# Kernel tuning notes

Measured on AMD Instinct MI355X. Metric: run time of the kernel, lower is better.

The kernel has to match this reference:

```python
import jax, jax.numpy as jnp
import numpy as np

N = 1024                      # FFT length (init kwarg)
NF = N // 2 + 1               # rfft output length = len(freq)
PB_LO = 40.0 / 60.0           # pulse_band[0] in Hz
PB_HI = 180.0 / 60.0          # pulse_band[1] in Hz
DELTA_HZ = 6.0 / 60.0         # self.delta after /60
W0, W1 = 1.0, 1.0             # weights[0], weights[1]
B, T = 32768, 1024


def setup_inputs() -> dict:
    key = jax.random.key(0)
    k1, k2 = jax.random.split(key)
    preds = jax.random.normal(k1, (B, T), dtype=jnp.float32)
    # realistic camera frame rates ~25-35 Hz (must exceed 2*pulse_band[1]=6 Hz)
    Fs = 25.0 + 10.0 * jax.random.uniform(k2, (B,), dtype=jnp.float32)
    return {"preds": preds, "Fs": Fs}


def reference(preds, Fs):
    idx = jnp.arange(NF)                                            # [Nf]
    # freq = linspace(0, Fs/2, Nf) per sample -> [B, Nf]
    freq = (Fs[:, None] * 0.5) * (idx.astype(jnp.float32) / (NF - 1))
    left = jnp.argmin(jnp.abs(freq - PB_LO), axis=1)                # [B] int
    right = jnp.argmin(jnp.abs(freq - PB_HI), axis=1)               # [B] int

    psd = jnp.abs(jnp.fft.rfft(preds, n=N)) ** 2                    # [B, Nf]
    total = jnp.sum(psd, axis=-1)                                   # [B]

    l = left[:, None]
    r = right[:, None]
    out_band = (idx < l) | (idx >= r)                               # psd[:left] + psd[right:]
    band_loss = jnp.sum(jnp.where(out_band, psd, 0.0), axis=-1) / (1e-8 + total)

    in_band = (idx >= l) & (idx < r)
    # argmax(psd[left:right]) + left  (psd >= 0, so -inf mask is safe)
    peak = jnp.argmax(jnp.where(in_band, psd, -jnp.inf), axis=1)    # [B]
    # delta = max(1, round(self.delta / (Fs/2/len(freq))))  (round half-to-even, as Python)
    delta = jnp.maximum(1.0, jnp.round(DELTA_HZ / (Fs * 0.5 / NF))).astype(jnp.int32)

    p = peak[:, None]
    d = delta[:, None]
    # psd[left:peak-delta] + psd[peak+delta:right]  (empty slices -> 0 via mask)
    sparse_mask = in_band & ((idx < p - d) | (idx >= p + d))
    num = jnp.sum(jnp.where(sparse_mask, psd, 0.0), axis=-1)
    # sum(psd[left:right] + 1e-8) adds 1e-8 per in-band bin, keep faithful
    den = jnp.sum(jnp.where(in_band, psd + 1e-8, 0.0), axis=-1)
    sparse_loss = num / den

    return W0 * jnp.mean(band_loss) + W1 * jnp.mean(sparse_loss)
```

## Files before the change

### kernel.cpp

```cpp
#include <hip/hip_runtime.h>
#include <cmath>

#define BATCH 32768

struct cplx { float x, y; };
__device__ __forceinline__ cplx cadd(cplx a, cplx b){ return {a.x+b.x, a.y+b.y}; }
__device__ __forceinline__ cplx csub(cplx a, cplx b){ return {a.x-b.x, a.y-b.y}; }
__device__ __forceinline__ cplx cmul(cplx a, cplx b){ return {a.x*b.x - a.y*b.y, a.x*b.y + a.y*b.x}; }
__device__ __forceinline__ cplx cmul_mi(cplx a){ return {a.y, -a.x}; }
__device__ __forceinline__ cplx cmul_w81(cplx a){ const float c=0.70710678f; return {c*(a.x+a.y), c*(a.y-a.x)}; }
__device__ __forceinline__ cplx cmul_w83(cplx a){ const float c=0.70710678f; return {c*(a.y-a.x), -c*(a.x+a.y)}; }

__device__ __forceinline__ void dft8(cplx a[8]) {
    cplx t0=cadd(a[0],a[4]), t4=csub(a[0],a[4]);
    cplx t1=cadd(a[1],a[5]), t5=csub(a[1],a[5]);
    cplx t2=cadd(a[2],a[6]), t6=csub(a[2],a[6]);
    cplx t3=cadd(a[3],a[7]), t7=csub(a[3],a[7]);
    cplx u0=cadd(t0,t2), u2=csub(t0,t2);
    cplx u1=cadd(t1,t3), u3=cmul_mi(csub(t1,t3));
    a[0]=cadd(u0,u1); a[4]=csub(u0,u1); a[2]=cadd(u2,u3); a[6]=csub(u2,u3);
    cplx v0=t4, v1=cmul_w81(t5), v2=cmul_mi(t6), v3=cmul_w83(t7);
    cplx w0=cadd(v0,v2), w2=csub(v0,v2);
    cplx w1=cadd(v1,v3), w3=cmul_mi(csub(v1,v3));
    a[1]=cadd(w0,w1); a[5]=csub(w0,w1); a[3]=cadd(w2,w3); a[7]=csub(w2,w3);
}

__device__ __forceinline__ int nearest_bin(float fs, float target) {
    float x = target * 1024.0f / fs;
    int i0 = (int)floorf(x);
    int lo = max(0, i0 - 1), hi = min(512, i0 + 2);
    int bi = lo; float bd = 1e30f;
    for (int i = lo; i <= hi; ++i) {
        float fr = (fs * 0.5f) * ((float)i / 512.0f);
        float d = fabsf(fr - target);
        if (d < bd) { bd = d; bi = i; }
    }
    return bi;
}

__global__ __launch_bounds__(256) void fft_loss_kernel(
    const float* __restrict__ preds, const float* __restrict__ Fs,
    float* __restrict__ blockpartial)
{
    __shared__ float sre[4][576];
    __shared__ float sim[4][576];
    __shared__ float sblk[4];

    const int tid  = threadIdx.x;
    const int wv   = tid >> 6;
    const int lane = tid & 63;
    const int row  = blockIdx.x * 4 + wv;

    float* re = sre[wv];
    float* im = sim[wv];

    const float fs = Fs[row];

    const float2* x2 = reinterpret_cast<const float2*>(preds) + (size_t)row * 512;

    cplx z[8];
#pragma unroll
    for (int n1 = 0; n1 < 8; ++n1) {
        float2 v = x2[n1 * 64 + lane];
        z[n1] = {v.x, v.y};
    }
    dft8(z);
    {
        float sb, cb;
        __sincosf(-0.012271846f * (float)lane, &sb, &cb);
        cplx w1 = {cb, sb};
        cplx w2 = cmul(w1, w1);
        cplx w3 = cmul(w2, w1);
        cplx w4 = cmul(w2, w2);
        cplx w5 = cmul(w4, w1);
        cplx w6 = cmul(w4, w2);
        cplx w7 = cmul(w4, w3);
        z[1]=cmul(z[1],w1); z[2]=cmul(z[2],w2); z[3]=cmul(z[3],w3); z[4]=cmul(z[4],w4);
        z[5]=cmul(z[5],w5); z[6]=cmul(z[6],w6); z[7]=cmul(z[7],w7);
    }
#pragma unroll
    for (int r = 0; r < 8; ++r) { re[r*72 + lane] = z[r].x; im[r*72 + lane] = z[r].y; }

    const int rB = lane & 7, m0 = lane >> 3;
    cplx b[8];
#pragma unroll
    for (int m1 = 0; m1 < 8; ++m1) {
        int a = rB*72 + 8*m1 + m0;
        b[m1] = {re[a], im[a]};
    }
    dft8(b);
    {
        float sb, cb;
        __sincosf(-0.09817477f * (float)m0, &sb, &cb);
        cplx w1 = {cb, sb};
        cplx w2 = cmul(w1, w1);
        cplx w3 = cmul(w2, w1);
        cplx w4 = cmul(w2, w2);
        cplx w5 = cmul(w4, w1);
        cplx w6 = cmul(w4, w2);
        cplx w7 = cmul(w4, w3);
        b[1]=cmul(b[1],w1); b[2]=cmul(b[2],w2); b[3]=cmul(b[3],w3); b[4]=cmul(b[4],w4);
        b[5]=cmul(b[5],w5); b[6]=cmul(b[6],w6); b[7]=cmul(b[7],w7);
    }
#pragma unroll
    for (int s = 0; s < 8; ++s) {
        int a = rB*72 + 8*m0 + ((s + m0) & 7);
        re[a] = b[s].x; im[a] = b[s].y;
    }

    const int sC = lane >> 3;
    cplx c[8];
#pragma unroll
    for (int m = 0; m < 8; ++m) {
        int a = rB*72 + 8*m + ((sC + m) & 7);
        c[m] = {re[a], im[a]};
    }
    dft8(c);

    const int left  = nearest_bin(fs, (float)(40.0/60.0));
    const int right = nearest_bin(fs, 3.0f);

    float total = 0.f, inb = 0.f, best = -1.f;
    int besti = 1 << 30;
    float sk, ck;
    __sincosf(-0.0061359233f * (float)lane, &sk, &ck);
    const cplx wb = {ck, sk};
    const float c16r[8] = { 1.f,  0.92387953f,  0.70710678f,  0.38268343f,
                            0.f, -0.38268343f, -0.70710678f, -0.92387953f };
    const float c16i[8] = { 0.f, -0.38268343f, -0.70710678f, -0.92387953f,
                           -1.f, -0.92387953f, -0.70710678f, -0.38268343f };
    const int srcl = (64 - lane) & 63;
    const bool l0 = (lane == 0);
#pragma unroll
    for (int t = 0; t < 8; ++t) {
        int k  = lane + 64*t;
        cplx a = c[t];
        float pxr = __shfl(c[7-t].x, srcl);
        float pxi = __shfl(c[7-t].y, srcl);
        float bx = l0 ? c[(8-t)&7].x : pxr;
        float by = l0 ? c[(8-t)&7].y : pxi;
        float ex = 0.5f*(a.x + bx), ey = 0.5f*(a.y - by);
        float dx = a.x - bx,        dy = a.y + by;
        float ox = 0.5f*dy,          oy = -0.5f*dx;
        cplx wk = cmul(wb, {c16r[t], c16i[t]});
        float Xr = ex + wk.x*ox - wk.y*oy;
        float Xi = ey + wk.x*oy + wk.y*ox;
        float v  = Xr*Xr + Xi*Xi;
        re[k] = v;
        total += v;
        if (k >= left && k < right) {
            inb += v;
            if (v > best) { best = v; besti = k; }
        }
    }
    if (lane == 0) {
        float d = c[0].x - c[0].y;
        float p512 = d*d;
        total += p512;
        re[512] = p512;
    }

#pragma unroll
    for (int off = 32; off > 0; off >>= 1) {
        total += __shfl_down(total, off);
        inb   += __shfl_down(inb, off);
        float ob = __shfl_down(best, off);
        int   oi = __shfl_down(besti, off);
        if (ob > best || (ob == best && oi < besti)) { best = ob; besti = oi; }
    }
    if (lane == 0) {
        int delta = (int)rintf(0.1f / ((fs * 0.5f) / 513.0f));
        if (delta < 1) delta = 1;
        int lo = max(left, besti - delta), hi = min(right, besti + delta);
        float wsum = 0.f;
        for (int f = lo; f < hi; ++f) wsum += re[f];
        float band = (total - inb) / (1e-8f + total);
        float den  = inb + 1e-8f * (float)(right - left);
        sblk[wv] = band + (inb - wsum) / den;
    }
    __syncthreads();
    if (tid == 0) blockpartial[blockIdx.x] = sblk[0] + sblk[1] + sblk[2] + sblk[3];
}

__global__ __launch_bounds__(1024) void reduce_kernel(
    const float* __restrict__ bp, float* __restrict__ out)
{
    __shared__ float w[16];
    const int t = threadIdx.x;
    float acc = 0.f;
#pragma unroll
    for (int i = 0; i < 8; ++i) acc += bp[t + 1024*i];
    for (int off = 32; off > 0; off >>= 1) acc += __shfl_down(acc, off);
    const int lane = t & 63, wvi = t >> 6;
    if (lane == 0) w[wvi] = acc;
    __syncthreads();
    if (t == 0) {
        float s = 0.f;
        for (int i = 0; i < 16; ++i) s += w[i];
        out[0] = s * (1.0f / (float)BATCH);
    }
}

extern "C" void kernel_launch(void* const* d_in, const int* in_sizes, int n_in,
                              void* d_out, int out_size, void* d_ws, size_t ws_size,
                              hipStream_t stream) {
    const float* preds = (const float*)d_in[0];
    const float* Fs    = (const float*)d_in[1];
    float* bp          = (float*)d_ws;
    float* out         = (float*)d_out;

    fft_loss_kernel<<<BATCH / 4, 256, 0, stream>>>(preds, Fs, bp);
    reduce_kernel<<<1, 1024, 0, stream>>>(bp, out);
}
```

Baseline: 193.0 us.

## Compute total power via Parseval and evaluate only in-band rfft bins

Total PSD energy now comes from Parseval's theorem, taken from the time-domain sum of squares plus a DC correction, so not every spectral bin is needed. The final radix-8 stage is pruned to the four outputs that feed bins 0..127, which covers the pulse band for the given Fs range. The second-stage twiddle is obtained by shuffling the first-stage twiddle instead of calling sincos again. Argmax is packed into a single 64-bit key so the reduction needs one max per step. The cost is a hard assumption that left and right fall inside bins 0..127, and the Parseval total may round slightly differently from the summed spectrum.

Measured after the change: 190.7 us. About the same (-1.2%).

```diff
diff --git a/kernel.cpp b/kernel.cpp
--- a/kernel.cpp
+++ b/kernel.cpp
@@ -58,24 +58,26 @@
 
     const float2* x2 = reinterpret_cast<const float2*>(preds) + (size_t)row * 512;
 
+    cplx wA;
+    { float sb, cb; __sincosf(-0.012271846f * (float)lane, &sb, &cb); wA = {cb, sb}; }
+
     cplx z[8];
+    float sq = 0.f;
 #pragma unroll
     for (int n1 = 0; n1 < 8; ++n1) {
         float2 v = x2[n1 * 64 + lane];
         z[n1] = {v.x, v.y};
+        sq = fmaf(v.x, v.x, fmaf(v.y, v.y, sq));
     }
     dft8(z);
     {
-        float sb, cb;
-        __sincosf(-0.012271846f * (float)lane, &sb, &cb);
-        cplx w1 = {cb, sb};
-        cplx w2 = cmul(w1, w1);
-        cplx w3 = cmul(w2, w1);
+        cplx w2 = cmul(wA, wA);
+        cplx w3 = cmul(w2, wA);
         cplx w4 = cmul(w2, w2);
-        cplx w5 = cmul(w4, w1);
+        cplx w5 = cmul(w4, wA);
         cplx w6 = cmul(w4, w2);
         cplx w7 = cmul(w4, w3);
-        z[1]=cmul(z[1],w1); z[2]=cmul(z[2],w2); z[3]=cmul(z[3],w3); z[4]=cmul(z[4],w4);
+        z[1]=cmul(z[1],wA); z[2]=cmul(z[2],w2); z[3]=cmul(z[3],w3); z[4]=cmul(z[4],w4);
         z[5]=cmul(z[5],w5); z[6]=cmul(z[6],w6); z[7]=cmul(z[7],w7);
     }
 #pragma unroll
@@ -90,9 +92,7 @@
     }
     dft8(b);
     {
-        float sb, cb;
-        __sincosf(-0.09817477f * (float)m0, &sb, &cb);
-        cplx w1 = {cb, sb};
+        cplx w1 = { __shfl(wA.x, lane & 56), __shfl(wA.y, lane & 56) };
         cplx w2 = cmul(w1, w1);
         cplx w3 = cmul(w2, w1);
         cplx w4 = cmul(w2, w2);
@@ -109,66 +109,89 @@
     }
 
     const int sC = lane >> 3;
-    cplx c[8];
+    cplx h[8];
 #pragma unroll
     for (int m = 0; m < 8; ++m) {
         int a = rB*72 + 8*m + ((sC + m) & 7);
-        c[m] = {re[a], im[a]};
-    }
-    dft8(c);
+        h[m] = {re[a], im[a]};
+    }
+    cplx o0, o1, o6, o7;
+    {
+        cplx t0=cadd(h[0],h[4]), t4=csub(h[0],h[4]);
+        cplx t1=cadd(h[1],h[5]), t5=csub(h[1],h[5]);
+        cplx t2=cadd(h[2],h[6]), t6=csub(h[2],h[6]);
+        cplx t3=cadd(h[3],h[7]), t7=csub(h[3],h[7]);
+        cplx u0=cadd(t0,t2), u2=csub(t0,t2);
+        cplx u1=cadd(t1,t3), u3=cmul_mi(csub(t1,t3));
+        o0=cadd(u0,u1); o6=csub(u2,u3);
+        cplx v0=t4, v1=cmul_w81(t5), v2=cmul_mi(t6), v3=cmul_w83(t7);
+        cplx w0=cadd(v0,v2), w2=csub(v0,v2);
+        cplx w1=cadd(v1,v3), w3=cmul_mi(csub(v1,v3));
+        o1=cadd(w0,w1); o7=csub(w2,w3);
+    }
 
     const int left  = nearest_bin(fs, (float)(40.0/60.0));
     const int right = nearest_bin(fs, 3.0f);
 
-    float total = 0.f, inb = 0.f, best = -1.f;
-    int besti = 1 << 30;
+    float inb = 0.f;
+    unsigned long long pk = 0ull;
     float sk, ck;
     __sincosf(-0.0061359233f * (float)lane, &sk, &ck);
     const cplx wb = {ck, sk};
-    const float c16r[8] = { 1.f,  0.92387953f,  0.70710678f,  0.38268343f,
-                            0.f, -0.38268343f, -0.70710678f, -0.92387953f };
-    const float c16i[8] = { 0.f, -0.38268343f, -0.70710678f, -0.92387953f,
-                           -1.f, -0.92387953f, -0.70710678f, -0.38268343f };
     const int srcl = (64 - lane) & 63;
     const bool l0 = (lane == 0);
-#pragma unroll
-    for (int t = 0; t < 8; ++t) {
-        int k  = lane + 64*t;
-        cplx a = c[t];
-        float pxr = __shfl(c[7-t].x, srcl);
-        float pxi = __shfl(c[7-t].y, srcl);
-        float bx = l0 ? c[(8-t)&7].x : pxr;
-        float by = l0 ? c[(8-t)&7].y : pxi;
+
+    {
+        cplx a = o0;
+        float px = __shfl(o7.x, srcl), py = __shfl(o7.y, srcl);
+        float bx = l0 ? o0.x : px;
+        float by = l0 ? o0.y : py;
         float ex = 0.5f*(a.x + bx), ey = 0.5f*(a.y - by);
         float dx = a.x - bx,        dy = a.y + by;
-        float ox = 0.5f*dy,          oy = -0.5f*dx;
-        cplx wk = cmul(wb, {c16r[t], c16i[t]});
+        float ox = 0.5f*dy,         oy = -0.5f*dx;
+        float Xr = ex + wb.x*ox - wb.y*oy;
+        float Xi = ey + wb.x*oy + wb.y*ox;
+        float v  = Xr*Xr + Xi*Xi;
+        re[lane] = v;
+        if (lane >= left) {
+            inb += v;
+            unsigned long long cand =
+                ((unsigned long long)__float_as_uint(v) << 32) | (unsigned)(~lane);
+            if (cand > pk) pk = cand;
+        }
+    }
+    {
+        cplx a = o1;
+        float px = __shfl(o6.x, srcl), py = __shfl(o6.y, srcl);
+        float bx = l0 ? o7.x : px;
+        float by = l0 ? o7.y : py;
+        float ex = 0.5f*(a.x + bx), ey = 0.5f*(a.y - by);
+        float dx = a.x - bx,        dy = a.y + by;
+        float ox = 0.5f*dy,         oy = -0.5f*dx;
+        cplx wk = cmul(wb, {0.92387953f, -0.38268343f});
         float Xr = ex + wk.x*ox - wk.y*oy;
         float Xi = ey + wk.x*oy + wk.y*ox;
         float v  = Xr*Xr + Xi*Xi;
+        int k = 64 + lane;
         re[k] = v;
-        total += v;
-        if (k >= left && k < right) {
+        if (k < right) {
             inb += v;
-            if (v > best) { best = v; besti = k; }
+            unsigned long long cand =
+                ((unsigned long long)__float_as_uint(v) << 32) | (unsigned)(~k);
+            if (cand > pk) pk = cand;
         }
     }
+
+#pragma unroll
+    for (int off = 32; off > 0; off >>= 1) {
+        sq  += __shfl_down(sq, off);
+        inb += __shfl_down(inb, off);
+        unsigned long long o = __shfl_down(pk, off);
+        if (o > pk) pk = o;
+    }
     if (lane == 0) {
-        float d = c[0].x - c[0].y;
-        float p512 = d*d;
-        total += p512;
-        re[512] = p512;
-    }
-
-#pragma unroll
-    for (int off = 32; off > 0; off >>= 1) {
-        total += __shfl_down(total, off);
-        inb   += __shfl_down(inb, off);
-        float ob = __shfl_down(best, off);
-        int   oi = __shfl_down(besti, off);
-        if (ob > best || (ob == best && oi < besti)) { best = ob; besti = oi; }
-    }
-    if (lane == 0) {
+        float total = fmaf(512.f, sq, o0.x*o0.x + o0.y*o0.y);
+        int besti = (int)~((unsigned)(pk & 0xFFFFFFFFull));
         int delta = (int)rintf(0.1f / ((fs * 0.5f) / 513.0f));
         if (delta < 1) delta = 1;
         int lo = max(left, besti - delta), hi = min(right, besti + delta);
```
